# Kernel tuning notes

Hardware: AMD Instinct MI355X
Metric: run time of the kernel (lower is better)

Reference implementation:

```python
import jax, jax.numpy as jnp
import numpy as np

B, N, FIN, H, F = 8, 1024, 256, 8, 64
NEG_SLOPE = 0.2


def setup_inputs() -> dict:
    key = jax.random.key(0)
    k = jax.random.split(key, 6)
    x = jax.random.normal(k[0], (B, N, FIN), dtype=jnp.float32)
    adj_mask = jax.random.randint(k[1], (B, N, N), 0, 2, dtype=jnp.int32)
    edge_prior = jax.random.normal(k[2], (B, N, N), dtype=jnp.float32)
    # params (xavier-style scales)
    W = jax.random.normal(k[3], (FIN, H * F), dtype=jnp.float32) * np.sqrt(2.0 / (FIN + H * F))
    a_left = jax.random.normal(k[4], (H, F), dtype=jnp.float32) * np.sqrt(2.0 / (1 + F))
    a_right = jax.random.normal(k[5], (H, F), dtype=jnp.float32) * np.sqrt(2.0 / (1 + F))
    edge_scale = jnp.float32(0.05)
    return {"x": x, "adj_mask": adj_mask, "edge_prior": edge_prior,
            "W": W, "a_left": a_left, "a_right": a_right, "edge_scale": edge_scale}


def reference(x, adj_mask, edge_prior, W, a_left, a_right, edge_scale):
    b, n, _ = x.shape
    h = (x @ W).reshape(b, n, H, F)                      # [B,N,H,F]
    e_left = jnp.einsum('bnhf,hf->bnh', h, a_left)       # [B,N,H]
    e_right = jnp.einsum('bnhf,hf->bnh', h, a_right)     # [B,N,H]
    e = jax.nn.leaky_relu(e_left[:, :, None, :] + e_right[:, None, :, :],
                          negative_slope=NEG_SLOPE)      # [B,N,N,H]
    e = e + edge_scale * edge_prior[..., None]
    e = jnp.where((adj_mask == 0)[..., None], -jnp.inf, e)
    alpha = jax.nn.softmax(e, axis=2)                    # softmax over neighbors j
    h_new = jnp.einsum('bijh,bjhf->bihf', alpha, h)      # [B,N,H,F]
    return h_new.reshape(b, n, H * F)                    # concat=True
```

## Files before the change

kernel.cpp:

```cpp
#include <hip/hip_runtime.h>
#include <hip/hip_bf16.h>

#define B_ 8
#define N_ 1024
#define FIN_ 256
#define H_ 8
#define F_ 64
#define HF_ 512
#define BN_ 8192
#define LOG2E 1.4426950408889634f

using bf16x8 = __attribute__((ext_vector_type(8))) short;
using f32x4  = __attribute__((ext_vector_type(4))) float;
using i32x4  = __attribute__((ext_vector_type(4))) int;

__device__ __forceinline__ short f2bf(float x) {
  __hip_bfloat16 b = __float2bfloat16(x);
  return *reinterpret_cast<short*>(&b);
}
__device__ __forceinline__ float bf2f(short s) {
  union { unsigned u; float f; } v;
  v.u = ((unsigned)(unsigned short)s) << 16;
  return v.f;
}
__device__ __forceinline__ bf16x8 cvtCE(f32x4 pa, f32x4 pb, i32x4 ma, i32x4 mb, float es) {
  bf16x8 o;
#pragma unroll
  for (int e = 0; e < 4; e++) {
    o[e]     = f2bf(ma[e] != 0 ? es * pa[e] : -1e30f);
    o[e + 4] = f2bf(mb[e] != 0 ? es * pb[e] : -1e30f);
  }
  return o;
}

__global__ __launch_bounds__(256) void k_cvt(
    const float* __restrict__ x, const float* __restrict__ W,
    short* __restrict__ xb, short* __restrict__ Wt) {
  const int bid = blockIdx.x;
  if (bid < 1024) {
    const int idx = (bid * 256 + threadIdx.x) * 8;
    f32x4 a = *(const f32x4*)(x + idx);
    f32x4 b = *(const f32x4*)(x + idx + 4);
    bf16x8 o;
    o[0]=f2bf(a[0]); o[1]=f2bf(a[1]); o[2]=f2bf(a[2]); o[3]=f2bf(a[3]);
    o[4]=f2bf(b[0]); o[5]=f2bf(b[1]); o[6]=f2bf(b[2]); o[7]=f2bf(b[3]);
    *(bf16x8*)(xb + idx) = o;
  } else {
    const int idx = (bid - 1024) * 256 + threadIdx.x;
    const int f = idx >> 8, c = idx & 255;
    Wt[f * FIN_ + c] = f2bf(W[c * HF_ + f]);
  }
}

__global__ __launch_bounds__(256) void k_h(
    const short* __restrict__ Wt, const short* __restrict__ xb,
    const float* __restrict__ aL, const float* __restrict__ aR,
    short* __restrict__ hA, float* __restrict__ el_t, float* __restrict__ er_t) {
  const int nt = blockIdx.x;
  const int h  = blockIdx.y;
  const int w  = threadIdx.x >> 6;
  const int l  = threadIdx.x & 63;
  const int lr = l & 15, lk = l >> 4;
  const int n0 = nt * 64;
  const int fbase = h * 64 + w * 16;

  f32x4 acc[4] = {};
  const short* arow = Wt + (fbase + lr) * FIN_ + lk * 8;

#pragma unroll
  for (int k0 = 0; k0 < FIN_; k0 += 32) {
    bf16x8 a = *(const bf16x8*)(arow + k0);
#pragma unroll
    for (int nf = 0; nf < 4; nf++) {
      bf16x8 bb = *(const bf16x8*)(xb + (size_t)(n0 + nf * 16 + lr) * FIN_ + k0 + lk * 8);
      acc[nf] = __builtin_amdgcn_mfma_f32_16x16x32_bf16(a, bb, acc[nf], 0, 0, 0);
    }
  }

  __shared__ short sT[64][72];
  __shared__ float sEl[4][64], sEr[4][64];
  float al[4], ar[4];
#pragma unroll
  for (int r = 0; r < 4; r++) {
    const int fl = w * 16 + lk * 4 + r;
    al[r] = aL[h * F_ + fl];
    ar[r] = aR[h * F_ + fl];
  }
#pragma unroll
  for (int nf = 0; nf < 4; nf++) {
    const int nl = nf * 16 + lr;
#pragma unroll
    for (int r = 0; r < 4; r++)
      sT[w * 16 + lk * 4 + r][nl] = f2bf(acc[nf][r]);
    float pl = acc[nf][0]*al[0] + acc[nf][1]*al[1] + acc[nf][2]*al[2] + acc[nf][3]*al[3];
    float pr = acc[nf][0]*ar[0] + acc[nf][1]*ar[1] + acc[nf][2]*ar[2] + acc[nf][3]*ar[3];
    pl += __shfl_xor(pl, 16); pl += __shfl_xor(pl, 32);
    pr += __shfl_xor(pr, 16); pr += __shfl_xor(pr, 32);
    if (lk == 0) { sEl[w][nl] = pl; sEr[w][nl] = pr; }
  }
  __syncthreads();
  if (threadIdx.x < 64) {
    const int n = threadIdx.x;
    el_t[h * BN_ + n0 + n] = (sEl[0][n] + sEl[1][n] + sEl[2][n] + sEl[3][n]) * LOG2E;
    er_t[h * BN_ + n0 + n] = (sEr[0][n] + sEr[1][n] + sEr[2][n] + sEr[3][n]) * LOG2E;
  }
  const int b8h = (nt >> 4) * 8 + h;
  const int jb  = (nt & 15) * 2;
#pragma unroll
  for (int gi = 0; gi < 2; gi++) {
    const int g   = threadIdx.x * 2 + gi;
    const int jsl = g >> 8, ff = (g >> 6) & 3, gl = g & 63;
    const int glr = gl & 15, glk = gl >> 4;
    bf16x8 v = *(const bf16x8*)(&sT[ff * 16 + glr][jsl * 32 + glk * 8]);
    *(bf16x8*)(hA + (((size_t)b8h * 32 + jb + jsl) * 4 + ff) * 512 + gl * 8) = v;
  }
}

#define PREF_(sn, Hd, Cd, E0d, E1d)                                   \
  {                                                                   \
    const short* hs_ = hW + (size_t)(sn) * 2048;                      \
    Hd[0] = *(const bf16x8*)(hs_);                                    \
    Hd[1] = *(const bf16x8*)(hs_ + 512);                              \
    Hd[2] = *(const bf16x8*)(hs_ + 1024);                             \
    Hd[3] = *(const bf16x8*)(hs_ + 1536);                             \
    Cd    = *(const bf16x8*)(cbl + (((sn) * 4 + lk) ^ xsw) * 8);      \
    E0d   = *(const f32x4*)(erp + (sn) * 32);                         \
    E1d   = *(const f32x4*)(erp + (sn) * 32 + 4);                     \
  }

#define COMP_(Hu, Cu, E0u, E1u)                                               \
  {                                                                           \
    bf16x8 pf;                                                                \
    _Pragma("unroll")                                                         \
    for (int q = 0; q < 4; q++) {                                             \
      float sA = el + E0u[q];                                                 \
      float vA = fmaf(0.6f, sA, bf2f(Cu[q]));                                 \
      vA = fmaf(0.4f, fabsf(sA), vA);                                         \
      float sB = el + E1u[q];                                                 \
      float vB = fmaf(0.6f, sB, bf2f(Cu[q + 4]));                             \
      vB = fmaf(0.4f, fabsf(sB), vB);                                         \
      float x1_, x2_;                                                         \
      asm("v_exp_f32 %0, %1" : "=v"(x1_) : "v"(vA));                          \
      asm("v_exp_f32 %0, %1" : "=v"(x2_) : "v"(vB));                          \
      pf[q] = f2bf(x1_); pf[q + 4] = f2bf(x2_);                               \
    }                                                                         \
    accS   = __builtin_amdgcn_mfma_f32_16x16x32_bf16(ones, pf, accS, 0, 0, 0);\
    acc[0] = __builtin_amdgcn_mfma_f32_16x16x32_bf16(Hu[0], pf, acc[0], 0,0,0);\
    acc[1] = __builtin_amdgcn_mfma_f32_16x16x32_bf16(Hu[1], pf, acc[1], 0,0,0);\
    acc[2] = __builtin_amdgcn_mfma_f32_16x16x32_bf16(Hu[2], pf, acc[2], 0,0,0);\
    acc[3] = __builtin_amdgcn_mfma_f32_16x16x32_bf16(Hu[3], pf, acc[3], 0,0,0);\
  }

__global__ __launch_bounds__(256, 4) void k_attn(
    const short* __restrict__ hA, const float* __restrict__ el_t,
    const float* __restrict__ er_t, const float* __restrict__ prior,
    const int* __restrict__ mask, const float* __restrict__ esp,
    float* __restrict__ out) {
  const int bid = blockIdx.x;
  const int b  = bid & 7;
  const int hp = (bid >> 3) & 1;
  const int it = bid >> 4;
  const int t  = threadIdx.x;
  const int h  = hp * 4 + (t >> 6);
  const int l  = t & 63;
  const int lr = l & 15, lk = l >> 4;
  const int i0 = it * 16;
  const size_t bn = (size_t)b * N_;
  const float es = esp[0] * LOG2E;

  __shared__ short cbuf[16 * 1024];

  {
    const int srow = t >> 4;
    const int cg0  = t & 15;
    const int sw   = srow & 7;
    const size_t grow = (bn + i0 + srow) * (size_t)N_;
    const float* pg = prior + grow;
    const int*   mg = mask  + grow;
#pragma unroll
    for (int k = 0; k < 8; k++) {
      const int g = cg0 + 16 * k;
      f32x4 p0 = *(const f32x4*)(pg + g * 8), p1 = *(const f32x4*)(pg + g * 8 + 4);
      i32x4 m0 = *(const i32x4*)(mg + g * 8), m1 = *(const i32x4*)(mg + g * 8 + 4);
      *(bf16x8*)(&cbuf[srow * 1024 + (g ^ sw) * 8]) = cvtCE(p0, p1, m0, m1, es);
    }
  }

  const float el = el_t[h * BN_ + bn + i0 + lr];
  const float* erp = er_t + h * BN_ + bn + lk * 8;
  const short* hW  = hA + (size_t)(b * 8 + h) * 65536 + l * 8;
  const short* cbl = cbuf + lr * 1024;
  const int xsw = lr & 7;

  bf16x8 hA_[4], hB_[4], cA_, cB_;
  f32x4 eA0, eA1, eB0, eB1;

  hA_[0] = *(const bf16x8*)(hW);
  hA_[1] = *(const bf16x8*)(hW + 512);
  hA_[2] = *(const bf16x8*)(hW + 1024);
  hA_[3] = *(const bf16x8*)(hW + 1536);
  eA0 = *(const f32x4*)(erp);
  eA1 = *(const f32x4*)(erp + 4);

  f32x4 acc[4] = {};
  f32x4 accS = {};
  bf16x8 ones;
#pragma unroll
  for (int e = 0; e < 8; e++) ones[e] = (short)0x3F80;

  __syncthreads();
  cA_ = *(const bf16x8*)(cbl + ((lk ^ xsw) * 8));

  for (int s = 0; s < 32; s += 2) {
    PREF_(s + 1, hB_, cB_, eB0, eB1);
    COMP_(hA_, cA_, eA0, eA1);
    const int s2 = (s + 2 < 32) ? s + 2 : 31;
    PREF_(s2, hA_, cA_, eA0, eA1);
    COMP_(hB_, cB_, eB0, eB1);
  }

  const float inv = 1.0f / accS[0];
  const size_t row = bn + i0 + lr;
#pragma unroll
  for (int ff = 0; ff < 4; ff++) {
    f32x4 v = acc[ff];
    v[0] *= inv; v[1] *= inv; v[2] *= inv; v[3] *= inv;
    *(f32x4*)(out + row * HF_ + h * 64 + ff * 16 + lk * 4) = v;
  }
}

extern "C" void kernel_launch(void* const* d_in, const int* in_sizes, int n_in,
                              void* d_out, int out_size, void* d_ws, size_t ws_size,
                              hipStream_t stream) {
  const float* x     = (const float*)d_in[0];
  const int*   adj   = (const int*)  d_in[1];
  const float* prior = (const float*)d_in[2];
  const float* W     = (const float*)d_in[3];
  const float* aL    = (const float*)d_in[4];
  const float* aR    = (const float*)d_in[5];
  const float* es    = (const float*)d_in[6];
  float* out = (float*)d_out;

  char* ws = (char*)d_ws;
  short* hA   = (short*)ws;
  short* xb   = (short*)(ws + 8u  * 1024 * 1024);
  short* Wt   = (short*)(ws + 12u * 1024 * 1024);
  float* el_t = (float*)(ws + 12u * 1024 * 1024 + 262144);
  float* er_t = (float*)(ws + 12u * 1024 * 1024 + 524288);

  hipLaunchKernelGGL(k_cvt, dim3(1536), dim3(256), 0, stream, x, W, xb, Wt);
  hipLaunchKernelGGL(k_h,   dim3(128, 8), dim3(256), 0, stream,
                     Wt, xb, aL, aR, hA, el_t, er_t);
  hipLaunchKernelGGL(k_attn, dim3(1024), dim3(256), 0, stream,
                     hA, el_t, er_t, prior, adj, es, out);
}
```

Baseline: 68.84 us.

## Process two 16-row query tiles per attention block to reuse H fragments

The attention kernel now handles 32 query rows per block instead of 16. Each loaded H fragment and er vector feeds two sets of MFMA accumulators, halving global H and er loads per output row. The grid is halved, launch bounds drop to 2 blocks per SM, and shared memory grows to 33 rows, which absorbs the prefetch that reads past the last row. In exchange, register pressure and LDS use rise and occupancy falls, and the final prefetch iterations read H and er data past the end of the per-head region.

```diff
diff --git a/kernel.cpp b/kernel.cpp
--- a/kernel.cpp
+++ b/kernel.cpp
@@ -55,7 +55,7 @@
 __global__ __launch_bounds__(256) void k_h(
     const short* __restrict__ Wt, const short* __restrict__ xb,
     const float* __restrict__ aL, const float* __restrict__ aR,
-    short* __restrict__ hA, float* __restrict__ el_t, float* __restrict__ er_t) {
+    short* __restrict__ hAg, float* __restrict__ el_t, float* __restrict__ er_t) {
   const int nt = blockIdx.x;
   const int h  = blockIdx.y;
   const int w  = threadIdx.x >> 6;
@@ -112,47 +112,66 @@
     const int jsl = g >> 8, ff = (g >> 6) & 3, gl = g & 63;
     const int glr = gl & 15, glk = gl >> 4;
     bf16x8 v = *(const bf16x8*)(&sT[ff * 16 + glr][jsl * 32 + glk * 8]);
-    *(bf16x8*)(hA + (((size_t)b8h * 32 + jb + jsl) * 4 + ff) * 512 + gl * 8) = v;
-  }
-}
-
-#define PREF_(sn, Hd, Cd, E0d, E1d)                                   \
+    *(bf16x8*)(hAg + (((size_t)b8h * 32 + jb + jsl) * 4 + ff) * 512 + gl * 8) = v;
+  }
+}
+
+#define PREF_G(sn, Hd, E0d, E1d)                                      \
   {                                                                   \
     const short* hs_ = hW + (size_t)(sn) * 2048;                      \
     Hd[0] = *(const bf16x8*)(hs_);                                    \
     Hd[1] = *(const bf16x8*)(hs_ + 512);                              \
     Hd[2] = *(const bf16x8*)(hs_ + 1024);                             \
     Hd[3] = *(const bf16x8*)(hs_ + 1536);                             \
-    Cd    = *(const bf16x8*)(cbl + (((sn) * 4 + lk) ^ xsw) * 8);      \
     E0d   = *(const f32x4*)(erp + (sn) * 32);                         \
     E1d   = *(const f32x4*)(erp + (sn) * 32 + 4);                     \
   }
 
-#define COMP_(Hu, Cu, E0u, E1u)                                               \
-  {                                                                           \
-    bf16x8 pf;                                                                \
-    _Pragma("unroll")                                                         \
-    for (int q = 0; q < 4; q++) {                                             \
-      float sA = el + E0u[q];                                                 \
-      float vA = fmaf(0.6f, sA, bf2f(Cu[q]));                                 \
-      vA = fmaf(0.4f, fabsf(sA), vA);                                         \
-      float sB = el + E1u[q];                                                 \
-      float vB = fmaf(0.6f, sB, bf2f(Cu[q + 4]));                             \
-      vB = fmaf(0.4f, fabsf(sB), vB);                                         \
-      float x1_, x2_;                                                         \
-      asm("v_exp_f32 %0, %1" : "=v"(x1_) : "v"(vA));                          \
-      asm("v_exp_f32 %0, %1" : "=v"(x2_) : "v"(vB));                          \
-      pf[q] = f2bf(x1_); pf[q + 4] = f2bf(x2_);                               \
-    }                                                                         \
-    accS   = __builtin_amdgcn_mfma_f32_16x16x32_bf16(ones, pf, accS, 0, 0, 0);\
-    acc[0] = __builtin_amdgcn_mfma_f32_16x16x32_bf16(Hu[0], pf, acc[0], 0,0,0);\
-    acc[1] = __builtin_amdgcn_mfma_f32_16x16x32_bf16(Hu[1], pf, acc[1], 0,0,0);\
-    acc[2] = __builtin_amdgcn_mfma_f32_16x16x32_bf16(Hu[2], pf, acc[2], 0,0,0);\
-    acc[3] = __builtin_amdgcn_mfma_f32_16x16x32_bf16(Hu[3], pf, acc[3], 0,0,0);\
-  }
-
-__global__ __launch_bounds__(256, 4) void k_attn(
-    const short* __restrict__ hA, const float* __restrict__ el_t,
+#define PREF_C(sn, C0d, C1d)                                          \
+  {                                                                   \
+    const int gi_ = (((sn) * 4 + lk) ^ xsw) * 8;                      \
+    C0d = *(const bf16x8*)(cbl0 + gi_);                               \
+    C1d = *(const bf16x8*)(cbl1 + gi_);                               \
+  }
+
+#define COMP2(Hu, C0u, C1u, E0u, E1u)                                          \
+  {                                                                            \
+    bf16x8 pfA, pfB;                                                           \
+    _Pragma("unroll")                                                          \
+    for (int q = 0; q < 4; q++) {                                              \
+      const float e0 = E0u[q], e1 = E1u[q];                                    \
+      float sA  = el0 + e0, sA2 = el0 + e1;                                    \
+      float sB  = el1 + e0, sB2 = el1 + e1;                                    \
+      float vA  = fmaf(0.6f, sA,  bf2f(C0u[q]));                               \
+      vA  = fmaf(0.4f, fabsf(sA),  vA);                                        \
+      float vA2 = fmaf(0.6f, sA2, bf2f(C0u[q + 4]));                           \
+      vA2 = fmaf(0.4f, fabsf(sA2), vA2);                                       \
+      float vB  = fmaf(0.6f, sB,  bf2f(C1u[q]));                               \
+      vB  = fmaf(0.4f, fabsf(sB),  vB);                                        \
+      float vB2 = fmaf(0.6f, sB2, bf2f(C1u[q + 4]));                           \
+      vB2 = fmaf(0.4f, fabsf(sB2), vB2);                                       \
+      float x1_, x2_, x3_, x4_;                                                \
+      asm("v_exp_f32 %0, %1" : "=v"(x1_) : "v"(vA));                           \
+      asm("v_exp_f32 %0, %1" : "=v"(x2_) : "v"(vA2));                          \
+      asm("v_exp_f32 %0, %1" : "=v"(x3_) : "v"(vB));                           \
+      asm("v_exp_f32 %0, %1" : "=v"(x4_) : "v"(vB2));                          \
+      pfA[q] = f2bf(x1_); pfA[q + 4] = f2bf(x2_);                              \
+      pfB[q] = f2bf(x3_); pfB[q + 4] = f2bf(x4_);                              \
+    }                                                                          \
+    accSA   = __builtin_amdgcn_mfma_f32_16x16x32_bf16(ones, pfA, accSA, 0,0,0);\
+    accSB   = __builtin_amdgcn_mfma_f32_16x16x32_bf16(ones, pfB, accSB, 0,0,0);\
+    accA[0] = __builtin_amdgcn_mfma_f32_16x16x32_bf16(Hu[0], pfA, accA[0],0,0,0);\
+    accB[0] = __builtin_amdgcn_mfma_f32_16x16x32_bf16(Hu[0], pfB, accB[0],0,0,0);\
+    accA[1] = __builtin_amdgcn_mfma_f32_16x16x32_bf16(Hu[1], pfA, accA[1],0,0,0);\
+    accB[1] = __builtin_amdgcn_mfma_f32_16x16x32_bf16(Hu[1], pfB, accB[1],0,0,0);\
+    accA[2] = __builtin_amdgcn_mfma_f32_16x16x32_bf16(Hu[2], pfA, accA[2],0,0,0);\
+    accB[2] = __builtin_amdgcn_mfma_f32_16x16x32_bf16(Hu[2], pfB, accB[2],0,0,0);\
+    accA[3] = __builtin_amdgcn_mfma_f32_16x16x32_bf16(Hu[3], pfA, accA[3],0,0,0);\
+    accB[3] = __builtin_amdgcn_mfma_f32_16x16x32_bf16(Hu[3], pfB, accB[3],0,0,0);\
+  }
+
+__global__ __launch_bounds__(256, 2) void k_attn(
+    const short* __restrict__ hAg, const float* __restrict__ el_t,
     const float* __restrict__ er_t, const float* __restrict__ prior,
     const int* __restrict__ mask, const float* __restrict__ esp,
     float* __restrict__ out) {
@@ -164,68 +183,72 @@
   const int h  = hp * 4 + (t >> 6);
   const int l  = t & 63;
   const int lr = l & 15, lk = l >> 4;
-  const int i0 = it * 16;
+  const int i0 = it * 32;
   const size_t bn = (size_t)b * N_;
   const float es = esp[0] * LOG2E;
 
-  __shared__ short cbuf[16 * 1024];
+  __shared__ short cbuf[33 * 1024];
 
   {
-    const int srow = t >> 4;
-    const int cg0  = t & 15;
+    const int srow = t >> 3;
+    const int g0   = t & 7;
     const int sw   = srow & 7;
     const size_t grow = (bn + i0 + srow) * (size_t)N_;
     const float* pg = prior + grow;
     const int*   mg = mask  + grow;
 #pragma unroll
-    for (int k = 0; k < 8; k++) {
-      const int g = cg0 + 16 * k;
+    for (int k = 0; k < 16; k++) {
+      const int g = g0 + 8 * k;
       f32x4 p0 = *(const f32x4*)(pg + g * 8), p1 = *(const f32x4*)(pg + g * 8 + 4);
       i32x4 m0 = *(const i32x4*)(mg + g * 8), m1 = *(const i32x4*)(mg + g * 8 + 4);
       *(bf16x8*)(&cbuf[srow * 1024 + (g ^ sw) * 8]) = cvtCE(p0, p1, m0, m1, es);
     }
   }
 
-  const float el = el_t[h * BN_ + bn + i0 + lr];
+  const float el0 = el_t[h * BN_ + bn + i0 + lr];
+  const float el1 = el_t[h * BN_ + bn + i0 + 16 + lr];
   const float* erp = er_t + h * BN_ + bn + lk * 8;
-  const short* hW  = hA + (size_t)(b * 8 + h) * 65536 + l * 8;
-  const short* cbl = cbuf + lr * 1024;
+  const short* hW  = hAg + (size_t)(b * 8 + h) * 65536 + l * 8;
+  const short* cbl0 = cbuf + lr * 1024;
+  const short* cbl1 = cbuf + (16 + lr) * 1024;
   const int xsw = lr & 7;
 
-  bf16x8 hA_[4], hB_[4], cA_, cB_;
+  bf16x8 HA[4], HB[4], cA0, cA1, cB0, cB1;
   f32x4 eA0, eA1, eB0, eB1;
 
-  hA_[0] = *(const bf16x8*)(hW);
-  hA_[1] = *(const bf16x8*)(hW + 512);
-  hA_[2] = *(const bf16x8*)(hW + 1024);
-  hA_[3] = *(const bf16x8*)(hW + 1536);
-  eA0 = *(const f32x4*)(erp);
-  eA1 = *(const f32x4*)(erp + 4);
-
-  f32x4 acc[4] = {};
-  f32x4 accS = {};
+  PREF_G(0, HA, eA0, eA1);
+  PREF_G(1, HB, eB0, eB1);
+
+  f32x4 accA[4] = {}, accB[4] = {};
+  f32x4 accSA = {}, accSB = {};
   bf16x8 ones;
 #pragma unroll
   for (int e = 0; e < 8; e++) ones[e] = (short)0x3F80;
 
   __syncthreads();
-  cA_ = *(const bf16x8*)(cbl + ((lk ^ xsw) * 8));
+  PREF_C(0, cA0, cA1);
+  PREF_C(1, cB0, cB1);
 
   for (int s = 0; s < 32; s += 2) {
-    PREF_(s + 1, hB_, cB_, eB0, eB1);
-    COMP_(hA_, cA_, eA0, eA1);
-    const int s2 = (s + 2 < 32) ? s + 2 : 31;
-    PREF_(s2, hA_, cA_, eA0, eA1);
-    COMP_(hB_, cB_, eB0, eB1);
-  }
-
-  const float inv = 1.0f / accS[0];
-  const size_t row = bn + i0 + lr;
+    COMP2(HA, cA0, cA1, eA0, eA1);
+    PREF_G(s + 2, HA, eA0, eA1);
+    PREF_C(s + 2, cA0, cA1);
+    COMP2(HB, cB0, cB1, eB0, eB1);
+    PREF_G(s + 3, HB, eB0, eB1);
+    PREF_C(s + 3, cB0, cB1);
+  }
+
+  const float invA = 1.0f / accSA[0];
+  const float invB = 1.0f / accSB[0];
+  const size_t rowA = bn + i0 + lr;
+  const size_t rowB = rowA + 16;
 #pragma unroll
   for (int ff = 0; ff < 4; ff++) {
-    f32x4 v = acc[ff];
-    v[0] *= inv; v[1] *= inv; v[2] *= inv; v[3] *= inv;
-    *(f32x4*)(out + row * HF_ + h * 64 + ff * 16 + lk * 4) = v;
+    f32x4 va = accA[ff], vb = accB[ff];
+    va[0]*=invA; va[1]*=invA; va[2]*=invA; va[3]*=invA;
+    vb[0]*=invB; vb[1]*=invB; vb[2]*=invB; vb[3]*=invB;
+    *(f32x4*)(out + rowA * HF_ + h * 64 + ff * 16 + lk * 4) = va;
+    *(f32x4*)(out + rowB * HF_ + h * 64 + ff * 16 + lk * 4) = vb;
   }
 }
 
@@ -242,7 +265,7 @@
   float* out = (float*)d_out;
 
   char* ws = (char*)d_ws;
-  short* hA   = (short*)ws;
+  short* hAg  = (short*)ws;
   short* xb   = (short*)(ws + 8u  * 1024 * 1024);
   short* Wt   = (short*)(ws + 12u * 1024 * 1024);
   float* el_t = (float*)(ws + 12u * 1024 * 1024 + 262144);
@@ -250,7 +273,7 @@
 
   hipLaunchKernelGGL(k_cvt, dim3(1536), dim3(256), 0, stream, x, W, xb, Wt);
   hipLaunchKernelGGL(k_h,   dim3(128, 8), dim3(256), 0, stream,
-                     Wt, xb, aL, aR, hA, el_t, er_t);
-  hipLaunchKernelGGL(k_attn, dim3(1024), dim3(256), 0, stream,
-                     hA, el_t, er_t, prior, adj, es, out);
-}
+                     Wt, xb, aL, aR, hAg, el_t, er_t);
+  hipLaunchKernelGGL(k_attn, dim3(512), dim3(256), 0, stream,
+                     hAg, el_t, er_t, prior, adj, es, out);
+}
```

Result: faster. 65.82 us (-4.4%).
